# Optimization experiments

Measured on AMD Instinct MI355X. Metric: run time of the kernel, lower is better.

The kernel has to match this reference:

```python
import jax, jax.numpy as jnp
import numpy as np

EMBED_DIM = 256
DIM_DYN = 64
BS = 8
NQ = 900
EPS = 1e-5


def layer_norm(x, gamma, beta, eps=EPS):
    mu = jnp.mean(x, axis=-1, keepdims=True)
    var = jnp.var(x, axis=-1, keepdims=True)
    return (x - mu) * jax.lax.rsqrt(var + eps) * gamma + beta


def setup_inputs() -> dict:
    key = jax.random.key(0)
    ks = jax.random.split(key, 8)
    E, D = EMBED_DIM, DIM_DYN
    np1 = 2 * E * D  # pre_dynamic_layer out dim (32768)
    np2 = E * D      # aft_dynamic_layer out dim (16384)
    s = 0.02
    return {
        "query": jax.random.normal(ks[0], (BS, NQ, E), jnp.float32),
        "sampled_feats": jax.random.normal(ks[1], (BS, NQ, 2 * E), jnp.float32),
        "W_pre": jax.random.normal(ks[2], (np1, E), jnp.float32) * s,
        "b_pre": jnp.zeros((np1,), jnp.float32),
        "W_aft": jax.random.normal(ks[3], (np2, E), jnp.float32) * s,
        "b_aft": jnp.zeros((np2,), jnp.float32),
        "W_out": jax.random.normal(ks[4], (E, E), jnp.float32) * s,
        "b_out": jnp.zeros((E,), jnp.float32),
        "g1": jnp.ones((D,), jnp.float32), "be1": jnp.zeros((D,), jnp.float32),
        "g2": jnp.ones((E,), jnp.float32), "be2": jnp.zeros((E,), jnp.float32),
        "g3": jnp.ones((E,), jnp.float32), "be3": jnp.zeros((E,), jnp.float32),
    }


def reference(query, sampled_feats, W_pre, b_pre, W_aft, b_aft, W_out, b_out,
              g1, be1, g2, be2, g3, be3):
    bs, nq, E = query.shape
    D = DIM_DYN
    B = bs * nq
    # features: (B, 1, 2E)
    feats = sampled_feats.reshape(B, 1, 2 * E)
    # per-query dynamic weights
    param1 = (query @ W_pre.T + b_pre).reshape(B, 2 * E, D)   # (B, 2E, D)
    param2 = (query @ W_aft.T + b_aft).reshape(B, D, E)       # (B, D, E)
    # tiny batched matmuls (1xK vectors)
    f = jnp.einsum('bik,bkd->bid', feats, param1)             # (B, 1, D)
    f = jax.nn.relu(layer_norm(f, g1, be1))
    f = jnp.einsum('bid,bde->bie', f, param2)                 # (B, 1, E)
    f = jax.nn.relu(layer_norm(f, g2, be2))
    # NOTE: original reshapes (bs*nq,1,E) -> (nq, bs, E), mixing batch/query order;
    # replicated faithfully.
    f = f.reshape(nq, bs, E)
    f = f @ W_out.T + b_out
    f = jax.nn.relu(layer_norm(f, g3, be3))
    return f
```

## Files before the change

### kernel.cpp

```cpp
#include <hip/hip_runtime.h>
#include <stdint.h>

#define BTOT 7200
#define EPSV 1e-5f

using bf16x8 = __attribute__((ext_vector_type(8))) __bf16;
using f32x4  = __attribute__((ext_vector_type(4))) float;


#define GLD16(gp, lp) __builtin_amdgcn_global_load_lds( \
    (const __attribute__((address_space(1))) uint32_t*)(gp), \
    (__attribute__((address_space(3))) uint32_t*)(lp), 16, 0, 0)

__device__ __forceinline__ void stage64k(char* ldsbase, const char* gsrc){
  const int w = (int)(threadIdx.x >> 6), lane = (int)(threadIdx.x & 63);
#pragma unroll
  for (int i = 0; i < 8; i++)
    GLD16(gsrc + i*8192 + w*1024 + lane*16, ldsbase + i*8192 + w*1024);
}

__global__ void prep_convert(const float* __restrict__ Wpre,
                             const float* __restrict__ Waft,
                             __bf16* __restrict__ dst)
{
  int g = (int)blockIdx.x * 256 + (int)threadIdx.x;
  const float* src;
  __bf16* d;
  if (g < 512*2048){ src = Wpre; d = dst; }
  else { g -= 512*2048; src = Waft; d = dst + (size_t)512*32768; }
  const int chunk = g >> 11, r = g & 2047;
  const int kb = r >> 6, j = r & 63;
  const float* sp = src + ((size_t)(chunk*64 + j))*256 + kb*8;
  float4 x0 = *(const float4*)sp;
  float4 x1 = *(const float4*)(sp + 4);
  float xs[8] = {x0.x,x0.y,x0.z,x0.w,x1.x,x1.y,x1.z,x1.w};
  bf16x8 hi, lo;
#pragma unroll
  for (int e = 0; e < 8; e++){
    __bf16 h = (__bf16)xs[e];
    hi[e] = h;
    lo[e] = (__bf16)(xs[e] - (float)h);
  }
  __bf16* base = d + (size_t)chunk*32768;
  *(bf16x8*)(base + r*8)        = hi;
  *(bf16x8*)(base + 16384 + r*8) = lo;
}

__global__ __launch_bounds__(512, 2) void stageA(
    const float* __restrict__ query, const float* __restrict__ feats,
    const float* __restrict__ b_pre, const __bf16* __restrict__ W,
    float* __restrict__ f1)
{
  __shared__ char lds[2*65536];
  const int bid = (int)blockIdx.x;
  const int js = bid & 3, bt = bid >> 2;
  const int b0 = bt * 128;
  const int w = (int)threadIdx.x >> 6, lane = (int)threadIdx.x & 63;
  const int l15 = lane & 15, l4 = lane >> 4;
  const int rtb = (w & 3) * 2;
  const int ch  = w >> 2;

  bf16x8 ahi[2][8], alo[2][8];
#pragma unroll
  for (int rt = 0; rt < 2; rt++){
    const int row = b0 + (rtb + rt)*16 + l15;
    const bool v = row < BTOT;
    const float* qp = query + (size_t)row*256 + l4*8;
#pragma unroll
    for (int ks = 0; ks < 8; ks++){
      float xs[8];
      if (v){
        float4 q0 = *(const float4*)(qp + ks*32);
        float4 q1 = *(const float4*)(qp + ks*32 + 4);
        xs[0]=q0.x; xs[1]=q0.y; xs[2]=q0.z; xs[3]=q0.w;
        xs[4]=q1.x; xs[5]=q1.y; xs[6]=q1.z; xs[7]=q1.w;
      } else {
#pragma unroll
        for (int e = 0; e < 8; e++) xs[e] = 0.f;
      }
#pragma unroll
      for (int e = 0; e < 8; e++){
        __bf16 h = (__bf16)xs[e];
        ahi[rt][ks][e] = h;
        alo[rt][ks][e] = (__bf16)(xs[e] - (float)h);
      }
    }
  }

  f32x4 acc[2][2] = {};
  const char* wbase = (const char*)(W + (size_t)(js*128)*32768);

  stage64k(lds, wbase);
  __syncthreads();

  for (int cc2 = 0; cc2 < 64; cc2++){
#pragma unroll
    for (int u = 0; u < 2; u++){
      const int cc = cc2*2 + u;
      if (cc < 127) stage64k(lds + (u^1)*65536, wbase + (size_t)(cc+1)*65536);
      const __bf16* bufh = (const __bf16*)(lds + u*65536);
      const __bf16* bufl = bufh + 16384;

      f32x4 c[2][2] = {};
#pragma unroll
      for (int ks = 0; ks < 8; ks++){
        bf16x8 bh[2], bl[2];
#pragma unroll
        for (int ct = 0; ct < 2; ct++){
          const int off = ((ks*4 + l4)*64 + ch*32 + ct*16 + l15) * 8;
          bh[ct] = *(const bf16x8*)(bufh + off);
          bl[ct] = *(const bf16x8*)(bufl + off);
        }
#pragma unroll
        for (int rt = 0; rt < 2; rt++)
#pragma unroll
          for (int ct = 0; ct < 2; ct++)
            c[rt][ct] = __builtin_amdgcn_mfma_f32_16x16x32_bf16(ahi[rt][ks], bh[ct], c[rt][ct], 0,0,0);
#pragma unroll
        for (int rt = 0; rt < 2; rt++)
#pragma unroll
          for (int ct = 0; ct < 2; ct++)
            c[rt][ct] = __builtin_amdgcn_mfma_f32_16x16x32_bf16(ahi[rt][ks], bl[ct], c[rt][ct], 0,0,0);
#pragma unroll
        for (int rt = 0; rt < 2; rt++)
#pragma unroll
          for (int ct = 0; ct < 2; ct++)
            c[rt][ct] = __builtin_amdgcn_mfma_f32_16x16x32_bf16(alo[rt][ks], bh[ct], c[rt][ct], 0,0,0);
      }

      const int k = js*128 + cc;
#pragma unroll
      for (int ct = 0; ct < 2; ct++){
        const int dcol = ch*32 + ct*16 + l15;
        const float bias = b_pre[k*64 + dcol];
#pragma unroll
        for (int rt = 0; rt < 2; rt++){
#pragma unroll
          for (int i = 0; i < 4; i++){
            const int row = b0 + (rtb + rt)*16 + l4*4 + i;
            const float wv = (row < BTOT) ? feats[(size_t)row*512 + k] : 0.f;
            acc[rt][ct][i] += wv * (c[rt][ct][i] + bias);
          }
        }
      }
      __syncthreads();
    }
  }

#pragma unroll
  for (int rt = 0; rt < 2; rt++)
#pragma unroll
    for (int ct = 0; ct < 2; ct++)
#pragma unroll
      for (int i = 0; i < 4; i++){
        const int row = b0 + (rtb + rt)*16 + l4*4 + i;
        if (row < BTOT){
          const int dcol = ch*32 + ct*16 + l15;
          atomicAdd(&f1[(size_t)row*64 + dcol], acc[rt][ct][i]);
        }
      }
}

__global__ __launch_bounds__(512, 2) void stageB(
    const float* __restrict__ query, const float* __restrict__ fln1,
    const float* __restrict__ b_aft, const __bf16* __restrict__ W,
    float* __restrict__ f2)
{
  __shared__ char lds[2*65536];
  const int bid = (int)blockIdx.x;
  const int js = bid & 1, bt = bid >> 1;
  const int b0 = bt * 64;
  const int w = (int)threadIdx.x >> 6, lane = (int)threadIdx.x & 63;
  const int l15 = lane & 15, l4 = lane >> 4;
  const int rt = w & 3;
  const int ch = w >> 2;

  bf16x8 ahi[8], alo[8];
  {
    const int row = b0 + rt*16 + l15;
    const bool v = row < BTOT;
    const float* qp = query + (size_t)row*256 + l4*8;
#pragma unroll
    for (int ks = 0; ks < 8; ks++){
      float xs[8];
      if (v){
        float4 q0 = *(const float4*)(qp + ks*32);
        float4 q1 = *(const float4*)(qp + ks*32 + 4);
        xs[0]=q0.x; xs[1]=q0.y; xs[2]=q0.z; xs[3]=q0.w;
        xs[4]=q1.x; xs[5]=q1.y; xs[6]=q1.z; xs[7]=q1.w;
      } else {
#pragma unroll
        for (int e = 0; e < 8; e++) xs[e] = 0.f;
      }
#pragma unroll
      for (int e = 0; e < 8; e++){
        __bf16 h = (__bf16)xs[e];
        ahi[ks][e] = h;
        alo[ks][e] = (__bf16)(xs[e] - (float)h);
      }
    }
  }

  f32x4 acc[4][2] = {};
  const char* wbase = (const char*)(W + (size_t)(js*128)*32768);

  stage64k(lds, wbase);
  __syncthreads();

  for (int cc4 = 0; cc4 < 32; cc4++){
#pragma unroll
    for (int q = 0; q < 4; q++){
      const int cc = cc4*4 + q;
      if (cc < 127) stage64k(lds + ((q&1)^1)*65536, wbase + (size_t)(cc+1)*65536);
      const __bf16* bufh = (const __bf16*)(lds + (q&1)*65536);
      const __bf16* bufl = bufh + 16384;

      f32x4 c0[2] = {}, c1[2] = {};
#pragma unroll
      for (int ks = 0; ks < 8; ks++){
        bf16x8 bh[2], bl[2];
#pragma unroll
        for (int ct = 0; ct < 2; ct++){
          const int off = ((ks*4 + l4)*64 + ch*32 + ct*16 + l15) * 8;
          bh[ct] = *(const bf16x8*)(bufh + off);
          bl[ct] = *(const bf16x8*)(bufl + off);
        }
#pragma unroll
        for (int ct = 0; ct < 2; ct++) c0[ct] = __builtin_amdgcn_mfma_f32_16x16x32_bf16(ahi[ks], bh[ct], c0[ct], 0,0,0);
#pragma unroll
        for (int ct = 0; ct < 2; ct++) c1[ct] = __builtin_amdgcn_mfma_f32_16x16x32_bf16(ahi[ks], bl[ct], c1[ct], 0,0,0);
#pragma unroll
        for (int ct = 0; ct < 2; ct++) c1[ct] = __builtin_amdgcn_mfma_f32_16x16x32_bf16(alo[ks], bh[ct], c1[ct], 0,0,0);
      }

      const int d = js*32 + cc4;
#pragma unroll
      for (int ct = 0; ct < 2; ct++){
        const int ecol = q*64 + ch*32 + ct*16 + l15;
        const float bias = b_aft[d*256 + ecol];
#pragma unroll
        for (int i = 0; i < 4; i++){
          const int row = b0 + rt*16 + l4*4 + i;
          const float wv = (row < BTOT) ? fln1[(size_t)row*64 + d] : 0.f;
          acc[q][ct][i] += wv * (c0[ct][i] + c1[ct][i] + bias);
        }
      }
      __syncthreads();
    }
  }

#pragma unroll
  for (int q = 0; q < 4; q++)
#pragma unroll
    for (int ct = 0; ct < 2; ct++)
#pragma unroll
      for (int i = 0; i < 4; i++){
        const int row = b0 + rt*16 + l4*4 + i;
        if (row < BTOT){
          const int e = q*64 + ch*32 + ct*16 + l15;
          atomicAdd(&f2[(size_t)row*256 + e], acc[q][ct][i]);
        }
      }
}

template<int WID>
__global__ void ln_relu(float* __restrict__ x, const float* __restrict__ gamma,
                        const float* __restrict__ beta)
{
  const int wv = (int)threadIdx.x >> 6, lane = (int)threadIdx.x & 63;
  const int row = (int)blockIdx.x*4 + wv;
  if (row >= BTOT) return;
  float* xr = x + (size_t)row * WID;
  constexpr int PER = WID / 64;
  float v[PER];
  if constexpr (PER == 1){
    v[0] = xr[lane];
  } else {
    float4 t = *(const float4*)(xr + lane*4);
    v[0]=t.x; v[1]=t.y; v[2]=t.z; v[3]=t.w;
  }
  float s = 0.f, sq = 0.f;
#pragma unroll
  for (int p = 0; p < PER; p++){ s += v[p]; sq += v[p]*v[p]; }
#pragma unroll
  for (int off = 32; off > 0; off >>= 1){
    s  += __shfl_xor(s, off);
    sq += __shfl_xor(sq, off);
  }
  const float mu = s * (1.f/WID);
  const float var = sq * (1.f/WID) - mu*mu;
  const float rs = rsqrtf(var + EPSV);
#pragma unroll
  for (int p = 0; p < PER; p++){
    const int col = (PER == 1) ? lane : lane*4 + p;
    const float y = (v[p] - mu)*rs*gamma[col] + beta[col];
    v[p] = fmaxf(y, 0.f);
  }
  if constexpr (PER == 1){ xr[lane] = v[0]; }
  else {
    float4 t; t.x=v[0]; t.y=v[1]; t.z=v[2]; t.w=v[3];
    *(float4*)(xr + lane*4) = t;
  }
}

__global__ __launch_bounds__(256) void stageC(
    const float* __restrict__ fln2, const float* __restrict__ Wout,
    const float* __restrict__ bout, const float* __restrict__ g3,
    const float* __restrict__ be3, float* __restrict__ out)
{
  __shared__ float xt[16][256];
  __shared__ float yt[16][256];
  const int t = (int)threadIdx.x;
  const int r0 = (int)blockIdx.x * 16;
#pragma unroll
  for (int i = 0; i < 16; i++) xt[i][t] = fln2[(size_t)(r0 + i)*256 + t];
  __syncthreads();
  const int lane = t & 63, wv = t >> 6;

  for (int ec = 0; ec < 4; ec++){
    const int e = ec*64 + lane;
    const float* wr = Wout + (size_t)e * 256;
    float a0=0.f, a1=0.f, a2=0.f, a3=0.f;
#pragma unroll 8
    for (int k4 = 0; k4 < 64; k4++){
      float4 wq = *(const float4*)(wr + k4*4);
      float4 x0 = *(const float4*)&xt[wv     ][k4*4];
      float4 x1 = *(const float4*)&xt[wv +  4][k4*4];
      float4 x2 = *(const float4*)&xt[wv +  8][k4*4];
      float4 x3 = *(const float4*)&xt[wv + 12][k4*4];
      a0 += x0.x*wq.x + x0.y*wq.y + x0.z*wq.z + x0.w*wq.w;
      a1 += x1.x*wq.x + x1.y*wq.y + x1.z*wq.z + x1.w*wq.w;
      a2 += x2.x*wq.x + x2.y*wq.y + x2.z*wq.z + x2.w*wq.w;
      a3 += x3.x*wq.x + x3.y*wq.y + x3.z*wq.z + x3.w*wq.w;
    }
    const float bb = bout[e];
    yt[wv     ][e] = a0 + bb;
    yt[wv +  4][e] = a1 + bb;
    yt[wv +  8][e] = a2 + bb;
    yt[wv + 12][e] = a3 + bb;
  }
  __syncthreads();

#pragma unroll
  for (int rr = 0; rr < 4; rr++){
    const int row = wv + rr*4;
    float4 v = *(const float4*)&yt[row][lane*4];
    float s  = v.x + v.y + v.z + v.w;
    float sq = v.x*v.x + v.y*v.y + v.z*v.z + v.w*v.w;
#pragma unroll
    for (int off = 32; off > 0; off >>= 1){
      s  += __shfl_xor(s, off);
      sq += __shfl_xor(sq, off);
    }
    const float mu = s * (1.f/256.f);
    const float var = sq * (1.f/256.f) - mu*mu;
    const float rs = rsqrtf(var + EPSV);
    const int c0 = lane*4;
    float4 o;
    o.x = fmaxf((v.x - mu)*rs*g3[c0  ] + be3[c0  ], 0.f);
    o.y = fmaxf((v.y - mu)*rs*g3[c0+1] + be3[c0+1], 0.f);
    o.z = fmaxf((v.z - mu)*rs*g3[c0+2] + be3[c0+2], 0.f);
    o.w = fmaxf((v.w - mu)*rs*g3[c0+3] + be3[c0+3], 0.f);
    *(float4*)(out + (size_t)(r0 + row)*256 + c0) = o;
  }
}

extern "C" void kernel_launch(void* const* d_in, const int* in_sizes, int n_in,
                              void* d_out, int out_size, void* d_ws, size_t ws_size,
                              hipStream_t stream)
{
  (void)in_sizes; (void)n_in; (void)out_size; (void)ws_size;
  const float* query = (const float*)d_in[0];
  const float* feats = (const float*)d_in[1];
  const float* Wpre  = (const float*)d_in[2];
  const float* bpre  = (const float*)d_in[3];
  const float* Waft  = (const float*)d_in[4];
  const float* baft  = (const float*)d_in[5];
  const float* Wout  = (const float*)d_in[6];
  const float* bout  = (const float*)d_in[7];
  const float* g1  = (const float*)d_in[8];
  const float* be1 = (const float*)d_in[9];
  const float* g2  = (const float*)d_in[10];
  const float* be2 = (const float*)d_in[11];
  const float* g3  = (const float*)d_in[12];
  const float* be3 = (const float*)d_in[13];
  float* outp = (float*)d_out;

  __bf16* wconv = (__bf16*)d_ws;
  float* f1 = (float*)((char*)d_ws + 50331648);
  float* f2 = (float*)((char*)d_ws + 52174848);

  hipMemsetAsync(f1, 0, 1843200 + 7372800, stream);
  prep_convert<<<6144, 256, 0, stream>>>(Wpre, Waft, wconv);
  stageA<<<228, 512, 0, stream>>>(query, feats, bpre, wconv, f1);
  ln_relu<64><<<1800, 256, 0, stream>>>(f1, g1, be1);
  stageB<<<226, 512, 0, stream>>>(query, f1, baft, wconv + (size_t)512*32768, f2);
  ln_relu<256><<<1800, 256, 0, stream>>>(f2, g2, be2);
  stageC<<<450, 256, 0, stream>>>(f2, Wout, bout, g3, be3, outp);
}
```

Measured before the change: 694.5 us.

## Restructure dynamic-weight stages with swizzled LDS, 6-deep pipeline, separate bias kernels

Replaces stageA/stageB with one templated kernel. It holds the query fragments in registers for 128 rows per wave group and streams 16KB swizzled weight units through a 6-slot LDS ring using a waitcnt-controlled pipeline and raised MFMA priority. The bias contributions move out into dedicated biasA and biasB kernels, which also initialise the outputs so the memset can be dropped. The goal is more MFMA work per loaded weight byte, fewer LDS bank conflicts and better overlap of loads with compute. The costs are two extra launches, higher register pressure and more atomics from the K-split.

```diff
diff --git a/kernel.cpp b/kernel.cpp
--- a/kernel.cpp
+++ b/kernel.cpp
@@ -6,74 +6,151 @@
 
 using bf16x8 = __attribute__((ext_vector_type(8))) __bf16;
 using f32x4  = __attribute__((ext_vector_type(4))) float;
-
 
 #define GLD16(gp, lp) __builtin_amdgcn_global_load_lds( \
     (const __attribute__((address_space(1))) uint32_t*)(gp), \
     (__attribute__((address_space(3))) uint32_t*)(lp), 16, 0, 0)
 
-__device__ __forceinline__ void stage64k(char* ldsbase, const char* gsrc){
-  const int w = (int)(threadIdx.x >> 6), lane = (int)(threadIdx.x & 63);
-#pragma unroll
-  for (int i = 0; i < 8; i++)
-    GLD16(gsrc + i*8192 + w*1024 + lane*16, ldsbase + i*8192 + w*1024);
-}
-
-__global__ void prep_convert(const float* __restrict__ Wpre,
-                             const float* __restrict__ Waft,
-                             __bf16* __restrict__ dst)
-{
-  int g = (int)blockIdx.x * 256 + (int)threadIdx.x;
-  const float* src;
-  __bf16* d;
-  if (g < 512*2048){ src = Wpre; d = dst; }
-  else { g -= 512*2048; src = Waft; d = dst + (size_t)512*32768; }
-  const int chunk = g >> 11, r = g & 2047;
-  const int kb = r >> 6, j = r & 63;
-  const float* sp = src + ((size_t)(chunk*64 + j))*256 + kb*8;
-  float4 x0 = *(const float4*)sp;
-  float4 x1 = *(const float4*)(sp + 4);
+__device__ __forceinline__ int swz(int d, int bir){ return (d*128 + bir) ^ ((d&7)<<4); }
+
+
+__global__ __launch_bounds__(256) void prep_convert(const float* __restrict__ Wpre,
+    const float* __restrict__ Waft, __bf16* __restrict__ dst)
+{
+  int g = (int)blockIdx.x*256 + (int)threadIdx.x;
+  const float* src; char* ubase; int sb;
+  if (g < 2048*512){
+    int u = g>>9, r = g&511;
+    int k = u>>2, eg = u&3, d = r>>3, oc = r&7;
+    src = Wpre + ((size_t)(k*64 + d))*256 + eg*64 + oc*8;
+    ubase = (char*)dst + (size_t)u*16384;
+    sb = swz(d, oc*16);
+  } else {
+    int g2 = g - 2048*512;
+    int u = g2>>9, r = g2&511;
+    int dd = u>>4, q = (u>>2)&3, eg = u&3, j = r>>3, oc = r&7;
+    src = Waft + ((size_t)(dd*256 + q*64 + j))*256 + eg*64 + oc*8;
+    ubase = (char*)dst + (size_t)(2048 + u)*16384;
+    sb = swz(j, oc*16);
+  }
+  float4 x0 = *(const float4*)src, x1 = *(const float4*)(src + 4);
   float xs[8] = {x0.x,x0.y,x0.z,x0.w,x1.x,x1.y,x1.z,x1.w};
   bf16x8 hi, lo;
 #pragma unroll
   for (int e = 0; e < 8; e++){
-    __bf16 h = (__bf16)xs[e];
-    hi[e] = h;
-    lo[e] = (__bf16)(xs[e] - (float)h);
-  }
-  __bf16* base = d + (size_t)chunk*32768;
-  *(bf16x8*)(base + r*8)        = hi;
-  *(bf16x8*)(base + 16384 + r*8) = lo;
-}
-
-__global__ __launch_bounds__(512, 2) void stageA(
-    const float* __restrict__ query, const float* __restrict__ feats,
-    const float* __restrict__ b_pre, const __bf16* __restrict__ W,
-    float* __restrict__ f1)
-{
-  __shared__ char lds[2*65536];
-  const int bid = (int)blockIdx.x;
-  const int js = bid & 3, bt = bid >> 2;
-  const int b0 = bt * 128;
-  const int w = (int)threadIdx.x >> 6, lane = (int)threadIdx.x & 63;
-  const int l15 = lane & 15, l4 = lane >> 4;
-  const int rtb = (w & 3) * 2;
-  const int ch  = w >> 2;
-
-  bf16x8 ahi[2][8], alo[2][8];
-#pragma unroll
-  for (int rt = 0; rt < 2; rt++){
-    const int row = b0 + (rtb + rt)*16 + l15;
-    const bool v = row < BTOT;
-    const float* qp = query + (size_t)row*256 + l4*8;
-#pragma unroll
-    for (int ks = 0; ks < 8; ks++){
+    __bf16 h = (__bf16)xs[e]; hi[e] = h; lo[e] = (__bf16)(xs[e] - (float)h);
+  }
+  *(bf16x8*)(ubase + sb) = hi;
+  *(bf16x8*)(ubase + 8192 + sb) = lo;
+}
+
+__global__ __launch_bounds__(256) void biasA(const float* __restrict__ feats,
+    const float* __restrict__ bp, float* __restrict__ f1)
+{
+  const int t = (int)threadIdx.x, d = t&63, bq = t>>6;
+  const int b0 = (int)blockIdx.x*32 + bq*8;
+  float acc[8] = {};
+  for (int k = 0; k < 512; k++){
+    float wv = bp[k*64 + d];
+#pragma unroll
+    for (int j = 0; j < 8; j++) acc[j] = fmaf(feats[(size_t)(b0+j)*512 + k], wv, acc[j]);
+  }
+#pragma unroll
+  for (int j = 0; j < 8; j++) f1[(size_t)(b0+j)*64 + d] = acc[j];
+}
+
+__global__ __launch_bounds__(1024) void biasB(const float* __restrict__ fln1,
+    const float* __restrict__ ba, float* __restrict__ f2)
+{
+  const int t = (int)threadIdx.x, eo = t&255, bq = t>>8;
+  const int b0 = (int)blockIdx.x*32 + bq*8;
+  float acc[8] = {};
+  for (int d = 0; d < 64; d++){
+    float wv = ba[d*256 + eo];
+#pragma unroll
+    for (int j = 0; j < 8; j++) acc[j] = fmaf(fln1[(size_t)(b0+j)*64 + d], wv, acc[j]);
+  }
+#pragma unroll
+  for (int j = 0; j < 8; j++) f2[(size_t)(b0+j)*256 + eo] = acc[j];
+}
+
+#define CHUNK_HALF(CI, WV) { \
+  asm volatile("s_waitcnt vmcnt(48)" ::: "memory"); \
+  __builtin_amdgcn_s_barrier(); \
+  asm volatile("" ::: "memory"); \
+  { const char* srcp = (const char*)Wu + (size_t)su*16384 + t*16; \
+    GLD16(srcp, &lds[sst]); GLD16(srcp + 8192, &lds[sst + 8192]); } \
+  if ((CI) + 6 < nch) su += ustep; \
+  sst += 16384; if (sst >= 98304) sst -= 98304; \
+  bf16x8 h0 = *(const bf16x8*)&lds[a00]; \
+  bf16x8 l0 = *(const bf16x8*)&lds[a01]; \
+  bf16x8 h1 = *(const bf16x8*)&lds[a10]; \
+  bf16x8 l1 = *(const bf16x8*)&lds[a11]; \
+  a00 += 16384; if (a00 >= 98304) a00 -= 98304; \
+  a01 += 16384; if (a01 >= 98304) a01 -= 98304; \
+  a10 += 16384; if (a10 >= 98304) a10 -= 98304; \
+  a11 += 16384; if (a11 >= 98304) a11 -= 98304; \
+  f32x4 c[8] = {}; \
+  __builtin_amdgcn_s_setprio(1); \
+  _Pragma("unroll") \
+  for (int bt = 0; bt < 8; bt++) c[bt] = __builtin_amdgcn_mfma_f32_16x16x32_bf16(h0, qh[bt][0], c[bt], 0,0,0); \
+  _Pragma("unroll") \
+  for (int bt = 0; bt < 8; bt++) c[bt] = __builtin_amdgcn_mfma_f32_16x16x32_bf16(h1, qh[bt][1], c[bt], 0,0,0); \
+  _Pragma("unroll") \
+  for (int bt = 0; bt < 8; bt++) c[bt] = __builtin_amdgcn_mfma_f32_16x16x32_bf16(h0, ql[bt][0], c[bt], 0,0,0); \
+  _Pragma("unroll") \
+  for (int bt = 0; bt < 8; bt++) c[bt] = __builtin_amdgcn_mfma_f32_16x16x32_bf16(h1, ql[bt][1], c[bt], 0,0,0); \
+  _Pragma("unroll") \
+  for (int bt = 0; bt < 8; bt++) c[bt] = __builtin_amdgcn_mfma_f32_16x16x32_bf16(l0, qh[bt][0], c[bt], 0,0,0); \
+  _Pragma("unroll") \
+  for (int bt = 0; bt < 8; bt++) c[bt] = __builtin_amdgcn_mfma_f32_16x16x32_bf16(l1, qh[bt][1], c[bt], 0,0,0); \
+  __builtin_amdgcn_s_setprio(0); \
+  { int wci = (CI) + 2; if (wci > nch-1) wci = nch-1; \
+    _Pragma("unroll") \
+    for (int bt = 0; bt < 8; bt++){ \
+      acc[bt] += WV[bt] * c[bt]; \
+      WV[bt] = wvsrc[rowc[bt] + wci]; } } }
+
+template<int STAGE>
+__global__ __launch_bounds__(512, 2) void stage_fused(
+    const float* __restrict__ query, const float* __restrict__ wvsrc,
+    const __bf16* __restrict__ Wu, float* __restrict__ outp)
+{
+  __shared__ __align__(16) char lds[98304];
+  const int t = (int)threadIdx.x, w = t>>6, lane = t&63, l15 = lane&15, l4 = lane>>4;
+  const int bg = w>>2, dg = w&3;
+
+  int eg, nch, ustep, uinit, wvstride, orow, ocol, wvoff;
+  if (STAGE == 0){
+    int sub = (int)blockIdx.x & 7; eg = sub>>1; int js = sub&1;
+    nch = 256; ustep = 4; uinit = js*1024 + eg;
+    wvstride = 512; wvoff = js*256; orow = 64; ocol = 0;
+  } else {
+    int sub = (int)blockIdx.x & 15; int qq = sub>>2; eg = sub&3;
+    nch = 64; ustep = 16; uinit = qq*4 + eg;
+    wvstride = 64; wvoff = 0; orow = 256; ocol = qq*64;
+  }
+  const int bt_ = (int)blockIdx.x >> (STAGE == 0 ? 3 : 4);
+  const int b0 = bt_*256 + bg*128;
+  const int eb = eg*64;
+
+  bf16x8 qh[8][2], ql[8][2];
+  int rowc[8];
+#pragma unroll
+  for (int bt = 0; bt < 8; bt++){
+    int b = b0 + bt*16 + l15;
+    bool v = b < BTOT;
+    int bc = v ? b : (BTOT-1);
+    rowc[bt] = bc*wvstride + wvoff;
+    const float* qp = query + (size_t)b*256 + eb + l4*8;
+#pragma unroll
+    for (int ks = 0; ks < 2; ks++){
       float xs[8];
       if (v){
-        float4 q0 = *(const float4*)(qp + ks*32);
-        float4 q1 = *(const float4*)(qp + ks*32 + 4);
-        xs[0]=q0.x; xs[1]=q0.y; xs[2]=q0.z; xs[3]=q0.w;
-        xs[4]=q1.x; xs[5]=q1.y; xs[6]=q1.z; xs[7]=q1.w;
+        float4 xa = *(const float4*)(qp + ks*32);
+        float4 xb = *(const float4*)(qp + ks*32 + 4);
+        xs[0]=xa.x; xs[1]=xa.y; xs[2]=xa.z; xs[3]=xa.w;
+        xs[4]=xb.x; xs[5]=xb.y; xs[6]=xb.z; xs[7]=xb.w;
       } else {
 #pragma unroll
         for (int e = 0; e < 8; e++) xs[e] = 0.f;
@@ -81,186 +158,52 @@
 #pragma unroll
       for (int e = 0; e < 8; e++){
         __bf16 h = (__bf16)xs[e];
-        ahi[rt][ks][e] = h;
-        alo[rt][ks][e] = (__bf16)(xs[e] - (float)h);
+        qh[bt][ks][e] = h;
+        ql[bt][ks][e] = (__bf16)(xs[e] - (float)h);
       }
     }
   }
 
-  f32x4 acc[2][2] = {};
-  const char* wbase = (const char*)(W + (size_t)(js*128)*32768);
-
-  stage64k(lds, wbase);
-  __syncthreads();
-
-  for (int cc2 = 0; cc2 < 64; cc2++){
-#pragma unroll
-    for (int u = 0; u < 2; u++){
-      const int cc = cc2*2 + u;
-      if (cc < 127) stage64k(lds + (u^1)*65536, wbase + (size_t)(cc+1)*65536);
-      const __bf16* bufh = (const __bf16*)(lds + u*65536);
-      const __bf16* bufl = bufh + 16384;
-
-      f32x4 c[2][2] = {};
-#pragma unroll
-      for (int ks = 0; ks < 8; ks++){
-        bf16x8 bh[2], bl[2];
-#pragma unroll
-        for (int ct = 0; ct < 2; ct++){
-          const int off = ((ks*4 + l4)*64 + ch*32 + ct*16 + l15) * 8;
-          bh[ct] = *(const bf16x8*)(bufh + off);
-          bl[ct] = *(const bf16x8*)(bufl + off);
-        }
-#pragma unroll
-        for (int rt = 0; rt < 2; rt++)
-#pragma unroll
-          for (int ct = 0; ct < 2; ct++)
-            c[rt][ct] = __builtin_amdgcn_mfma_f32_16x16x32_bf16(ahi[rt][ks], bh[ct], c[rt][ct], 0,0,0);
-#pragma unroll
-        for (int rt = 0; rt < 2; rt++)
-#pragma unroll
-          for (int ct = 0; ct < 2; ct++)
-            c[rt][ct] = __builtin_amdgcn_mfma_f32_16x16x32_bf16(ahi[rt][ks], bl[ct], c[rt][ct], 0,0,0);
-#pragma unroll
-        for (int rt = 0; rt < 2; rt++)
-#pragma unroll
-          for (int ct = 0; ct < 2; ct++)
-            c[rt][ct] = __builtin_amdgcn_mfma_f32_16x16x32_bf16(alo[rt][ks], bh[ct], c[rt][ct], 0,0,0);
-      }
-
-      const int k = js*128 + cc;
-#pragma unroll
-      for (int ct = 0; ct < 2; ct++){
-        const int dcol = ch*32 + ct*16 + l15;
-        const float bias = b_pre[k*64 + dcol];
-#pragma unroll
-        for (int rt = 0; rt < 2; rt++){
-#pragma unroll
-          for (int i = 0; i < 4; i++){
-            const int row = b0 + (rtb + rt)*16 + l4*4 + i;
-            const float wv = (row < BTOT) ? feats[(size_t)row*512 + k] : 0.f;
-            acc[rt][ct][i] += wv * (c[rt][ct][i] + bias);
-          }
-        }
-      }
-      __syncthreads();
-    }
-  }
-
-#pragma unroll
-  for (int rt = 0; rt < 2; rt++)
-#pragma unroll
-    for (int ct = 0; ct < 2; ct++)
-#pragma unroll
-      for (int i = 0; i < 4; i++){
-        const int row = b0 + (rtb + rt)*16 + l4*4 + i;
-        if (row < BTOT){
-          const int dcol = ch*32 + ct*16 + l15;
-          atomicAdd(&f1[(size_t)row*64 + dcol], acc[rt][ct][i]);
-        }
-      }
-}
-
-__global__ __launch_bounds__(512, 2) void stageB(
-    const float* __restrict__ query, const float* __restrict__ fln1,
-    const float* __restrict__ b_aft, const __bf16* __restrict__ W,
-    float* __restrict__ f2)
-{
-  __shared__ char lds[2*65536];
-  const int bid = (int)blockIdx.x;
-  const int js = bid & 1, bt = bid >> 1;
-  const int b0 = bt * 64;
-  const int w = (int)threadIdx.x >> 6, lane = (int)threadIdx.x & 63;
-  const int l15 = lane & 15, l4 = lane >> 4;
-  const int rt = w & 3;
-  const int ch = w >> 2;
-
-  bf16x8 ahi[8], alo[8];
-  {
-    const int row = b0 + rt*16 + l15;
-    const bool v = row < BTOT;
-    const float* qp = query + (size_t)row*256 + l4*8;
-#pragma unroll
-    for (int ks = 0; ks < 8; ks++){
-      float xs[8];
-      if (v){
-        float4 q0 = *(const float4*)(qp + ks*32);
-        float4 q1 = *(const float4*)(qp + ks*32 + 4);
-        xs[0]=q0.x; xs[1]=q0.y; xs[2]=q0.z; xs[3]=q0.w;
-        xs[4]=q1.x; xs[5]=q1.y; xs[6]=q1.z; xs[7]=q1.w;
-      } else {
-#pragma unroll
-        for (int e = 0; e < 8; e++) xs[e] = 0.f;
-      }
-#pragma unroll
-      for (int e = 0; e < 8; e++){
-        __bf16 h = (__bf16)xs[e];
-        ahi[ks][e] = h;
-        alo[ks][e] = (__bf16)(xs[e] - (float)h);
-      }
-    }
-  }
-
-  f32x4 acc[4][2] = {};
-  const char* wbase = (const char*)(W + (size_t)(js*128)*32768);
-
-  stage64k(lds, wbase);
-  __syncthreads();
-
-  for (int cc4 = 0; cc4 < 32; cc4++){
-#pragma unroll
-    for (int q = 0; q < 4; q++){
-      const int cc = cc4*4 + q;
-      if (cc < 127) stage64k(lds + ((q&1)^1)*65536, wbase + (size_t)(cc+1)*65536);
-      const __bf16* bufh = (const __bf16*)(lds + (q&1)*65536);
-      const __bf16* bufl = bufh + 16384;
-
-      f32x4 c0[2] = {}, c1[2] = {};
-#pragma unroll
-      for (int ks = 0; ks < 8; ks++){
-        bf16x8 bh[2], bl[2];
-#pragma unroll
-        for (int ct = 0; ct < 2; ct++){
-          const int off = ((ks*4 + l4)*64 + ch*32 + ct*16 + l15) * 8;
-          bh[ct] = *(const bf16x8*)(bufh + off);
-          bl[ct] = *(const bf16x8*)(bufl + off);
-        }
-#pragma unroll
-        for (int ct = 0; ct < 2; ct++) c0[ct] = __builtin_amdgcn_mfma_f32_16x16x32_bf16(ahi[ks], bh[ct], c0[ct], 0,0,0);
-#pragma unroll
-        for (int ct = 0; ct < 2; ct++) c1[ct] = __builtin_amdgcn_mfma_f32_16x16x32_bf16(ahi[ks], bl[ct], c1[ct], 0,0,0);
-#pragma unroll
-        for (int ct = 0; ct < 2; ct++) c1[ct] = __builtin_amdgcn_mfma_f32_16x16x32_bf16(alo[ks], bh[ct], c1[ct], 0,0,0);
-      }
-
-      const int d = js*32 + cc4;
-#pragma unroll
-      for (int ct = 0; ct < 2; ct++){
-        const int ecol = q*64 + ch*32 + ct*16 + l15;
-        const float bias = b_aft[d*256 + ecol];
-#pragma unroll
-        for (int i = 0; i < 4; i++){
-          const int row = b0 + rt*16 + l4*4 + i;
-          const float wv = (row < BTOT) ? fln1[(size_t)row*64 + d] : 0.f;
-          acc[q][ct][i] += wv * (c0[ct][i] + c1[ct][i] + bias);
-        }
-      }
-      __syncthreads();
-    }
-  }
-
-#pragma unroll
-  for (int q = 0; q < 4; q++)
-#pragma unroll
-    for (int ct = 0; ct < 2; ct++)
-#pragma unroll
-      for (int i = 0; i < 4; i++){
-        const int row = b0 + rt*16 + l4*4 + i;
-        if (row < BTOT){
-          const int e = q*64 + ch*32 + ct*16 + l15;
-          atomicAdd(&f2[(size_t)row*256 + e], acc[q][ct][i]);
-        }
-      }
+  int a00 = swz(dg*16 + l15, l4*16);
+  int a01 = a00 + 8192;
+  int a10 = swz(dg*16 + l15, 64 + l4*16);
+  int a11 = a10 + 8192;
+  int sst = 5*16384 + t*16;
+  int su  = uinit;
+
+  f32x4 acc[8] = {};
+  float wvA[8], wvB[8];
+
+#pragma unroll
+  for (int j = 0; j < 5; j++){
+    const char* srcp = (const char*)Wu + (size_t)su*16384 + t*16;
+    GLD16(srcp, &lds[j*16384 + t*16]);
+    GLD16(srcp + 8192, &lds[j*16384 + 8192 + t*16]);
+    su += ustep;
+    int wci = (j-3 < 0) ? 0 : (j-3);
+    if (((j+1)&1) == 0){
+#pragma unroll
+      for (int bt = 0; bt < 8; bt++) wvA[bt] = wvsrc[rowc[bt] + wci];
+    } else {
+#pragma unroll
+      for (int bt = 0; bt < 8; bt++) wvB[bt] = wvsrc[rowc[bt] + wci];
+    }
+  }
+
+  for (int ci = 0; ci < nch; ci += 2){
+    CHUNK_HALF(ci,   wvA)
+    CHUNK_HALF(ci+1, wvB)
+  }
+
+#pragma unroll
+  for (int bt = 0; bt < 8; bt++){
+    int b = b0 + bt*16 + l15;
+    if (b < BTOT){
+      float* op = outp + (size_t)b*orow + ocol + dg*16 + l4*4;
+#pragma unroll
+      for (int i = 0; i < 4; i++) atomicAdd(op + i, acc[bt][i]);
+    }
+  }
 }
 
 template<int WID>
@@ -276,8 +219,8 @@
   if constexpr (PER == 1){
     v[0] = xr[lane];
   } else {
-    float4 t = *(const float4*)(xr + lane*4);
-    v[0]=t.x; v[1]=t.y; v[2]=t.z; v[3]=t.w;
+    float4 tq = *(const float4*)(xr + lane*4);
+    v[0]=tq.x; v[1]=tq.y; v[2]=tq.z; v[3]=tq.w;
   }
   float s = 0.f, sq = 0.f;
 #pragma unroll
@@ -298,8 +241,8 @@
   }
   if constexpr (PER == 1){ xr[lane] = v[0]; }
   else {
-    float4 t; t.x=v[0]; t.y=v[1]; t.z=v[2]; t.w=v[3];
-    *(float4*)(xr + lane*4) = t;
+    float4 tq; tq.x=v[0]; tq.y=v[1]; tq.z=v[2]; tq.w=v[3];
+    *(float4*)(xr + lane*4) = tq;
   }
 }
 
@@ -390,11 +333,12 @@
   float* f1 = (float*)((char*)d_ws + 50331648);
   float* f2 = (float*)((char*)d_ws + 52174848);
 
-  hipMemsetAsync(f1, 0, 1843200 + 7372800, stream);
   prep_convert<<<6144, 256, 0, stream>>>(Wpre, Waft, wconv);
-  stageA<<<228, 512, 0, stream>>>(query, feats, bpre, wconv, f1);
+  biasA<<<225, 256, 0, stream>>>(feats, bpre, f1);
+  stage_fused<0><<<232, 512, 0, stream>>>(query, feats, wconv, f1);
   ln_relu<64><<<1800, 256, 0, stream>>>(f1, g1, be1);
-  stageB<<<226, 512, 0, stream>>>(query, f1, baft, wconv + (size_t)512*32768, f2);
+  biasB<<<225, 1024, 0, stream>>>(f1, baft, f2);
+  stage_fused<1><<<464, 512, 0, stream>>>(query, f1, wconv + (size_t)2048*8192, f2);
   ln_relu<256><<<1800, 256, 0, stream>>>(f2, g2, be2);
   stageC<<<450, 256, 0, stream>>>(f2, Wout, bout, g3, be3, outp);
 }
```

Measured after the change: 1.436 ms. +106.7%, slower.
